# Performance work log

Measured on AMD Instinct MI355X. Metric: run time of the kernel, lower is better.

The kernel has to match this reference:

```python
import jax, jax.numpy as jnp
import numpy as np

N_NODES = 10000
N_EDGES = 320000
NODE_C = 256
IN_EDGE_C = 256
OUT_EDGE_C = 512
BN_EPS = 1e-5


def setup_inputs() -> dict:
    key = jax.random.key(0)
    ks = jax.random.split(key, 10)
    d_in = 2 * NODE_C + IN_EDGE_C  # 768
    x = jax.random.normal(ks[0], (N_NODES, NODE_C), dtype=jnp.float32)
    edge_index = jax.random.randint(ks[1], (2, N_EDGES), 0, N_NODES, dtype=jnp.int64)
    edge_attr = jax.random.normal(ks[2], (N_EDGES, IN_EDGE_C), dtype=jnp.float32)
    # MLP params (Linear stored as [in, out] for x @ W + b)
    W1 = jax.random.normal(ks[3], (d_in, OUT_EDGE_C), dtype=jnp.float32) / np.sqrt(d_in)
    b1 = jnp.zeros((OUT_EDGE_C,), dtype=jnp.float32)
    W2 = jax.random.normal(ks[4], (OUT_EDGE_C, OUT_EDGE_C), dtype=jnp.float32) / np.sqrt(OUT_EDGE_C)
    b2 = jnp.zeros((OUT_EDGE_C,), dtype=jnp.float32)
    # BatchNorm affine params
    gamma = jnp.ones((OUT_EDGE_C,), dtype=jnp.float32)
    beta = jnp.zeros((OUT_EDGE_C,), dtype=jnp.float32)
    return {"x": x, "edge_index": edge_index, "edge_attr": edge_attr,
            "W1": W1, "b1": b1, "W2": W2, "b2": b2,
            "gamma": gamma, "beta": beta}


def reference(x, edge_index, edge_attr, W1, b1, W2, b2, gamma, beta):
    src = edge_index[0]  # x_j (source / neighbor)
    dst = edge_index[1]  # x_i (target, aggregation index)
    x_i = x[dst]                                  # [E, node_c]
    x_j = x[src]                                  # [E, node_c]
    m = jnp.concatenate([x_i, x_j - x_i, edge_attr], axis=-1)  # [E, 2*node_c+edge_c]
    h = jax.nn.relu(m @ W1 + b1) @ W2 + b2        # per-edge MLP -> [E, out_c]
    out = jax.ops.segment_sum(h, dst, num_segments=x.shape[0])  # scatter-add -> [N, out_c]
    # BatchNorm1d (training-mode batch statistics, biased variance)
    mean = jnp.mean(out, axis=0)
    var = jnp.var(out, axis=0)
    y = (out - mean) * jax.lax.rsqrt(var + BN_EPS) * gamma + beta
    return jax.nn.relu(y)
```

## Files before the change

kernel.cpp:

```cpp
#include <hip/hip_runtime.h>
#include <hip/hip_bf16.h>
#include <cstdint>

#define NN 10000
#define NE 320000
#define NC 256
#define OC 512
#define K1 256

typedef __bf16 bf16_t;
typedef bf16_t bf16x8 __attribute__((ext_vector_type(8)));
typedef bf16_t bf16x4 __attribute__((ext_vector_type(4)));
typedef bf16_t bf16x2 __attribute__((ext_vector_type(2)));
typedef float  f32x4  __attribute__((ext_vector_type(4)));
typedef float  f32x2  __attribute__((ext_vector_type(2)));

__device__ __forceinline__ void gload_lds16(const void* g, void* l) {
  __builtin_amdgcn_global_load_lds(
      (const __attribute__((address_space(1))) unsigned int*)g,
      (__attribute__((address_space(3))) unsigned int*)l, 16, 0, 0);
}

__device__ __forceinline__ int permB(int R) {
  return (R & ~63) + ((R & 15) << 2) + ((R >> 4) & 3);
}
__device__ __forceinline__ int permB32(int R) {
  return (R & ~31) + ((R & 15) << 1) + ((R >> 4) & 1);
}

__global__ void k_prep(const float* __restrict__ x,
                       const float* __restrict__ W1,
                       const float* __restrict__ W2,
                       bf16_t* __restrict__ xb,
                       bf16_t* __restrict__ w1abt,
                       bf16_t* __restrict__ w1ct,
                       bf16_t* __restrict__ w2t,
                       float* __restrict__ agg,
                       int* __restrict__ deg,
                       int* __restrict__ cursor,
                       float* __restrict__ sums) {
  const int stride = gridDim.x * blockDim.x;
  for (int i = blockIdx.x * blockDim.x + threadIdx.x; i < NN * OC; i += stride) {
    agg[i] = 0.0f;
    if (i < NN * NC) xb[i] = (bf16_t)x[i];
    if (i < 1024 * K1) {
      const int n = i >> 8, k = i & 255;
      float w;
      if (n < OC) w = W1[(size_t)k * OC + n] - W1[(size_t)(k + NC) * OC + n];
      else        w = W1[(size_t)(k + NC) * OC + (n - OC)];
      w1abt[i] = (bf16_t)w;
    }
    if (i < OC * K1) {
      const int n = i >> 8, k = i & 255;
      w1ct[i] = (bf16_t)W1[(size_t)(512 + k) * OC + n];
    }
    if (i < OC * OC) {
      const int n = i >> 9, k = i & 511;
      w2t[i] = (bf16_t)W2[(size_t)k * OC + n];
    }
    if (i < NN) { deg[i] = 0; cursor[i] = 0; }
    if (i < 1024) sums[i] = 0.0f;
  }
}

__global__ void k_deg(const int* __restrict__ dstIdx, int* __restrict__ deg) {
  const int i = blockIdx.x * blockDim.x + threadIdx.x;
  if (i < NE) atomicAdd(&deg[dstIdx[i]], 1);
}

__global__ void k_scan(const int* __restrict__ deg, int* __restrict__ offs) {
  __shared__ int carry;
  __shared__ int wsum[4];
  if (threadIdx.x == 0) carry = 0;
  __syncthreads();
  const int lane = threadIdx.x & 63, w = threadIdx.x >> 6;
  for (int base = 0; base < NN; base += 256) {
    const int i = base + threadIdx.x;
    const int v = (i < NN) ? deg[i] : 0;
    int s = v;
#pragma unroll
    for (int d = 1; d < 64; d <<= 1) { int t = __shfl_up(s, d); if (lane >= d) s += t; }
    if (lane == 63) wsum[w] = s;
    __syncthreads();
    int woff = 0;
    for (int j = 0; j < w; j++) woff += wsum[j];
    const int incl = s + woff + carry;
    if (i < NN) offs[i] = incl - v;
    __syncthreads();
    if (threadIdx.x == 255) carry = incl;
    __syncthreads();
  }
}

__global__ void k_scatter(const int* __restrict__ srcIdx, const int* __restrict__ dstIdx,
                          const int* __restrict__ offs, int* __restrict__ cursor,
                          int* __restrict__ eperm, int* __restrict__ sdst,
                          int* __restrict__ ssrc) {
  const int e = blockIdx.x * blockDim.x + threadIdx.x;
  if (e < NE) {
    const int d = dstIdx[e];
    const int pos = offs[d] + atomicAdd(&cursor[d], 1);
    eperm[pos] = e;
    sdst[pos] = d;
    ssrc[pos] = srcIdx[e];
  }
}

__global__ __launch_bounds__(256) void k_pq(
    const bf16_t* __restrict__ xb,
    const bf16_t* __restrict__ w1abt,
    const float*  __restrict__ b1,
    float*        __restrict__ P,
    bf16_t*       __restrict__ Qb) {
  __shared__ bf16_t sA[128 * 64];
  __shared__ bf16_t sB[128 * 64];

  const int tid = threadIdx.x;
  const int cb = blockIdx.x & 7, rblk = blockIdx.x >> 3;
  const int r0 = rblk * 128, n0 = cb * 128;
  const int lane = tid & 63, wid = tid >> 6;
  const int mbase = (wid >> 1) * 64, nbase = (wid & 1) * 64;
  const int lr = lane >> 3, ls = lane & 7, slog = ls ^ lr;
  const int g = lane >> 4;

  f32x4 acc[4][4];
#pragma unroll
  for (int mi = 0; mi < 4; mi++)
#pragma unroll
    for (int ni = 0; ni < 4; ni++) acc[mi][ni] = (f32x4){0.f, 0.f, 0.f, 0.f};

  for (int kb = 0; kb < K1; kb += 64) {
#pragma unroll
    for (int i = 0; i < 4; i++) {
      const int row = wid * 32 + i * 8;
      int grow = r0 + row + lr;
      if (grow > NN - 1) grow = NN - 1;
      gload_lds16(xb + (size_t)grow * NC + kb + slog * 8, &sA[row * 64]);
      gload_lds16(w1abt + (size_t)(n0 + permB(row + lr)) * K1 + kb + slog * 8,
                  &sB[row * 64]);
    }
    __syncthreads();
#pragma unroll
    for (int kk = 0; kk < 2; kk++) {
      const int sl = kk * 4 + g;
      bf16x8 av[4], bv[4];
#pragma unroll
      for (int mi = 0; mi < 4; mi++) {
        const int rA = mbase + mi * 16 + (lane & 15);
        av[mi] = *(const bf16x8*)&sA[rA * 64 + ((sl ^ (rA & 7)) * 8)];
      }
#pragma unroll
      for (int ni = 0; ni < 4; ni++) {
        const int rB = nbase + ni * 16 + (lane & 15);
        bv[ni] = *(const bf16x8*)&sB[rB * 64 + ((sl ^ (rB & 7)) * 8)];
      }
#pragma unroll
      for (int mi = 0; mi < 4; mi++)
#pragma unroll
        for (int ni = 0; ni < 4; ni++)
          acc[mi][ni] = __builtin_amdgcn_mfma_f32_16x16x32_bf16(av[mi], bv[ni], acc[mi][ni], 0, 0, 0);
    }
    __syncthreads();
  }

  const int col0 = n0 + nbase + (lane & 15) * 4;
  f32x4 b1v = {0.f, 0.f, 0.f, 0.f};
  if (col0 < OC) b1v = *(const f32x4*)&b1[col0];
#pragma unroll
  for (int mi = 0; mi < 4; mi++) {
#pragma unroll
    for (int q = 0; q < 4; q++) {
      const int grow = r0 + mbase + mi * 16 + g * 4 + q;
      if (grow < NN) {
        if (col0 < OC) {
          f32x4 v;
#pragma unroll
          for (int j = 0; j < 4; j++) v[j] = acc[mi][j][q] + b1v[j];
          *(f32x4*)&P[(size_t)grow * OC + col0] = v;
        } else {
          bf16x4 v;
#pragma unroll
          for (int j = 0; j < 4; j++) v[j] = (bf16_t)acc[mi][j][q];
          *(bf16x4*)&Qb[(size_t)grow * OC + (col0 - OC)] = v;
        }
      }
    }
  }
}

__global__ __launch_bounds__(512, 4) void k_edge_gemm(
    const float*  __restrict__ ea,
    const bf16_t* __restrict__ w1ct,
    const float*  __restrict__ P,
    const bf16_t* __restrict__ Qb,
    const int*    __restrict__ eperm,
    const int*    __restrict__ sdst,
    const int*    __restrict__ ssrc,
    float*        __restrict__ agg) {
  __shared__ bf16_t sM[2][128 * 64];
  __shared__ bf16_t sW[2][128 * 64];
  __shared__ int sDst[128];
  __shared__ int sSrc[128];
  __shared__ int sE[128];

  const int bid = (blockIdx.x & 7) * 1250 + (blockIdx.x >> 3);
  const int cb = bid & 3, eblk = bid >> 2;
  const int e0 = eblk * 128, n0 = cb * 128;

  const int tid = threadIdx.x;
  if (tid < 128) {
    sDst[tid] = sdst[e0 + tid];
    sSrc[tid] = ssrc[e0 + tid];
    sE[tid]   = eperm[e0 + tid];
  }
  __syncthreads();

  const int lane = tid & 63, wid = tid >> 6;
  const int mbase = (wid >> 2) * 64;
  const int nbase = (wid & 3) * 32;
  const int g = lane >> 4, r = lane & 15;
  const int lr = lane >> 3, ls = lane & 7, slogW = ls ^ lr;
  const int mrow = tid >> 2, qd = tid & 3;
  const int msw = mrow & 7;
  const float* eaRow = ea + (size_t)sE[mrow] * NC;

#define STAGE_W(kt, b)                                                        \
  _Pragma("unroll") for (int i = 0; i < 2; i++) {                             \
    const int rowb = wid * 16 + i * 8;       \
    gload_lds16(w1ct + (size_t)(n0 + permB32(rowb + lr)) * K1 + (kt)*64 + slogW * 8, \
                &sW[b][rowb * 64]);                                           \
  }
#define LOAD_A(kt)                                                            \
  _Pragma("unroll") for (int j = 0; j < 4; j++)                               \
      a[j] = *(const f32x4*)(eaRow + (kt)*64 + qd * 16 + j * 4);
#define WRITE_M(b)                                                            \
  _Pragma("unroll") for (int tt = 0; tt < 2; tt++) {                          \
    const int slot = qd * 2 + tt;                                             \
    bf16x8 v;                                                                 \
    _Pragma("unroll") for (int jj = 0; jj < 4; jj++) {                        \
      v[jj] = (bf16_t)a[tt * 2][jj];                                          \
      v[4 + jj] = (bf16_t)a[tt * 2 + 1][jj];                                  \
    }                                                                         \
    *(bf16x8*)&sM[b][mrow * 64 + ((slot ^ msw) * 8)] = v;                     \
  }

  f32x4 a[4];
  STAGE_W(0, 0);
  LOAD_A(0);
  WRITE_M(0);

  f32x4 acc[4][2];
#pragma unroll
  for (int mi = 0; mi < 4; mi++)
#pragma unroll
    for (int ni = 0; ni < 2; ni++) acc[mi][ni] = (f32x4){0.f, 0.f, 0.f, 0.f};

#pragma unroll
  for (int t = 0; t < 4; t++) {
    const int b = t & 1;
    __syncthreads();
    if (t < 3) { STAGE_W(t + 1, b ^ 1); LOAD_A(t + 1); }
#pragma unroll
    for (int kk = 0; kk < 2; kk++) {
      const int sl = kk * 4 + g;
      bf16x8 av[4], bv[2];
#pragma unroll
      for (int mi = 0; mi < 4; mi++) {
        const int rA = mbase + mi * 16 + r;
        av[mi] = *(const bf16x8*)&sM[b][rA * 64 + ((sl ^ (rA & 7)) * 8)];
      }
#pragma unroll
      for (int ni = 0; ni < 2; ni++) {
        const int rB = nbase + ni * 16 + r;
        bv[ni] = *(const bf16x8*)&sW[b][rB * 64 + ((sl ^ (rB & 7)) * 8)];
      }
#pragma unroll
      for (int mi = 0; mi < 4; mi++)
#pragma unroll
        for (int ni = 0; ni < 2; ni++)
          acc[mi][ni] = __builtin_amdgcn_mfma_f32_16x16x32_bf16(av[mi], bv[ni], acc[mi][ni], 0, 0, 0);
    }
    if (t < 3) { WRITE_M(b ^ 1); }
  }
#undef STAGE_W
#undef LOAD_A
#undef WRITE_M

  const int col0 = n0 + nbase + r * 2;
#pragma unroll
  for (int mi = 0; mi < 4; mi++) {
    const int rbase = mbase + mi * 16 + g * 4;
    const int d0 = sDst[rbase],     d1 = sDst[rbase + 1];
    const int d2 = sDst[rbase + 2], d3 = sDst[rbase + 3];
    const int s0 = sSrc[rbase],     s1 = sSrc[rbase + 1];
    const int s2 = sSrc[rbase + 2], s3 = sSrc[rbase + 3];
    const int headId = d0, tailId = d3;
    const bool b1q = (d1 != d0), b2q = (d2 != d1), b3q = (d3 != d2);
    const bool seen = b1q | b2q | b3q;
    bool match[3];
#pragma unroll
    for (int j = 0; j < 3; j++) {
      const int tIdj = __shfl(tailId, (lane & 15) | (j << 4));
      match[j] = (j < g) && (tIdj == headId);
    }
    const int nextHead = __shfl(headId, (lane + 16) & 63);
    const bool endsHere = (g == 3) || (nextHead != tailId);

    const f32x2 P0 = *(const f32x2*)&P[(size_t)d0 * OC + col0];
    const f32x2 P1 = *(const f32x2*)&P[(size_t)d1 * OC + col0];
    const f32x2 P2 = *(const f32x2*)&P[(size_t)d2 * OC + col0];
    const f32x2 P3 = *(const f32x2*)&P[(size_t)d3 * OC + col0];
    const bf16x2 Q0 = *(const bf16x2*)&Qb[(size_t)s0 * OC + col0];
    const bf16x2 Q1 = *(const bf16x2*)&Qb[(size_t)s1 * OC + col0];
    const bf16x2 Q2 = *(const bf16x2*)&Qb[(size_t)s2 * OC + col0];
    const bf16x2 Q3 = *(const bf16x2*)&Qb[(size_t)s3 * OC + col0];

    f32x2 v0, v1, v2, v3;
#pragma unroll
    for (int j = 0; j < 2; j++) {
      v0[j] = fmaxf(acc[mi][j][0] + P0[j] + (float)Q0[j], 0.f);
      v1[j] = fmaxf(acc[mi][j][1] + P1[j] + (float)Q1[j], 0.f);
      v2[j] = fmaxf(acc[mi][j][2] + P2[j] + (float)Q2[j], 0.f);
      v3[j] = fmaxf(acc[mi][j][3] + P3[j] + (float)Q3[j], 0.f);
    }

    f32x2 head = {0.f, 0.f}, run = v0;
    bool first = true;
    if (b1q) { head = run; first = false; run = v1; } else run += v1;
    if (b2q) {
      if (first) { head = run; first = false; }
      else {
        float* base = agg + (size_t)d1 * OC + col0;
#pragma unroll
        for (int j = 0; j < 2; j++) if (run[j] != 0.f) atomicAdd(base + j, run[j]);
      }
      run = v2;
    } else run += v2;
    if (b3q) {
      if (first) { head = run; first = false; }
      else {
        float* base = agg + (size_t)d2 * OC + col0;
#pragma unroll
        for (int j = 0; j < 2; j++) if (run[j] != 0.f) atomicAdd(base + j, run[j]);
      }
      run = v3;
    } else run += v3;
    const f32x2 tailSum = run;

    f32x2 inc = {0.f, 0.f};
#pragma unroll
    for (int jg = 0; jg < 3; jg++) {
      f32x2 ts;
#pragma unroll
      for (int c = 0; c < 2; c++) ts[c] = __shfl(tailSum[c], (lane & 15) | (jg << 4));
      if (match[jg]) inc += ts;
    }
    if (seen) {
      float* base = agg + (size_t)headId * OC + col0;
#pragma unroll
      for (int j = 0; j < 2; j++) {
        const float h = head[j] + inc[j];
        if (h != 0.f) atomicAdd(base + j, h);
      }
    }
    if (endsHere) {
      float* base = agg + (size_t)tailId * OC + col0;
#pragma unroll
      for (int j = 0; j < 2; j++) {
        const float t2 = tailSum[j] + (seen ? 0.f : inc[j]);
        if (t2 != 0.f) atomicAdd(base + j, t2);
      }
    }
  }
}

__global__ __launch_bounds__(256) void k_node_gemm(
    const float*  __restrict__ agg,
    const bf16_t* __restrict__ w2t,
    const float*  __restrict__ b2,
    const int*    __restrict__ deg,
    float*        __restrict__ out,
    float*        __restrict__ sums) {
  __shared__ bf16_t sM[128 * 72];
  __shared__ bf16_t sW[128 * 72];

  const int tid  = threadIdx.x;
  const int bid  = blockIdx.x;
  const int cb   = bid & 3;
  const int rblk = bid >> 2;
  const int r0   = rblk * 128;
  const int n0   = cb * 128;

  const int lane  = tid & 63, wid = tid >> 6;
  const int mbase = (wid >> 1) * 64, nbase = (wid & 1) * 64;
  const int se = tid >> 1;
  const int sk = (tid & 1) * 32;
  const int arow  = r0 + se;
  const bool rowok = arow < NN;

  f32x4 acc[4][4];
#pragma unroll
  for (int mi = 0; mi < 4; mi++)
#pragma unroll
    for (int ni = 0; ni < 4; ni++) acc[mi][ni] = (f32x4){0.f, 0.f, 0.f, 0.f};

  for (int kb = 0; kb < OC; kb += 64) {
    {
      bf16x8* dst = (bf16x8*)&sM[se * 72 + sk];
      if (rowok) {
        const float* pf = agg + (size_t)arow * OC + kb + sk;
        f32x4 f[8];
#pragma unroll
        for (int i = 0; i < 8; i++) f[i] = *(const f32x4*)(pf + i * 4);
#pragma unroll
        for (int i = 0; i < 4; i++) {
          bf16x8 v;
#pragma unroll
          for (int j = 0; j < 4; j++) {
            v[j]     = (bf16_t)f[2 * i][j];
            v[4 + j] = (bf16_t)f[2 * i + 1][j];
          }
          dst[i] = v;
        }
      } else {
        bf16x8 z = {};
        dst[0] = z; dst[1] = z; dst[2] = z; dst[3] = z;
      }
    }
    {
      const bf16_t* pw = w2t + (size_t)(n0 + permB(se)) * OC + kb + sk;
      bf16x8* dst = (bf16x8*)&sW[se * 72 + sk];
      dst[0] = *(const bf16x8*)(pw);
      dst[1] = *(const bf16x8*)(pw + 8);
      dst[2] = *(const bf16x8*)(pw + 16);
      dst[3] = *(const bf16x8*)(pw + 24);
    }
    __syncthreads();
#pragma unroll
    for (int kk = 0; kk < 2; kk++) {
      const int krd = kk * 32 + (lane >> 4) * 8;
      bf16x8 av[4], bv[4];
#pragma unroll
      for (int mi = 0; mi < 4; mi++)
        av[mi] = *(const bf16x8*)&sM[(mbase + mi * 16 + (lane & 15)) * 72 + krd];
#pragma unroll
      for (int ni = 0; ni < 4; ni++)
        bv[ni] = *(const bf16x8*)&sW[(nbase + ni * 16 + (lane & 15)) * 72 + krd];
#pragma unroll
      for (int mi = 0; mi < 4; mi++)
#pragma unroll
        for (int ni = 0; ni < 4; ni++)
          acc[mi][ni] = __builtin_amdgcn_mfma_f32_16x16x32_bf16(av[mi], bv[ni], acc[mi][ni], 0, 0, 0);
    }
    __syncthreads();
  }

  const int col0 = n0 + nbase + (lane & 15) * 4;
  const f32x4 b2v = *(const f32x4*)&b2[col0];
  const int g = lane >> 4;
  f32x4 s1 = {0.f, 0.f, 0.f, 0.f}, s2 = {0.f, 0.f, 0.f, 0.f};
#pragma unroll
  for (int mi = 0; mi < 4; mi++) {
#pragma unroll
    for (int q = 0; q < 4; q++) {
      const int row = r0 + mbase + mi * 16 + g * 4 + q;
      if (row < NN) {
        const float dg = (float)deg[row];
        f32x4 v;
#pragma unroll
        for (int j = 0; j < 4; j++) {
          v[j] = acc[mi][j][q] + b2v[j] * dg;
          s1[j] += v[j];
          s2[j] += v[j] * v[j];
        }
        *(f32x4*)&out[(size_t)row * OC + col0] = v;
      }
    }
  }
#pragma unroll
  for (int j = 0; j < 4; j++) {
    s1[j] += __shfl_xor(s1[j], 16);  s2[j] += __shfl_xor(s2[j], 16);
    s1[j] += __shfl_xor(s1[j], 32);  s2[j] += __shfl_xor(s2[j], 32);
  }
  if (g == 0) {
#pragma unroll
    for (int j = 0; j < 4; j++) {
      atomicAdd(&sums[col0 + j], s1[j]);
      atomicAdd(&sums[OC + col0 + j], s2[j]);
    }
  }
}

__global__ void k_bn_apply(float* __restrict__ out,
                           const float* __restrict__ sums,
                           const float* __restrict__ gamma,
                           const float* __restrict__ beta) {
  const int i = blockIdx.x * blockDim.x + threadIdx.x;
  f32x4 v = *((const f32x4*)out + i);
  const int c = (i & 127) << 2;
  const f32x4 sm = *(const f32x4*)&sums[c];
  const f32x4 sq = *(const f32x4*)&sums[OC + c];
  const f32x4 gm = *(const f32x4*)&gamma[c];
  const f32x4 bt = *(const f32x4*)&beta[c];
  f32x4 r;
#pragma unroll
  for (int j = 0; j < 4; j++) {
    const float mean = sm[j] * (1.0f / NN);
    const float var  = sq[j] * (1.0f / NN) - mean * mean;
    const float sc   = rsqrtf(var + 1e-5f) * gm[j];
    r[j] = fmaxf(v[j] * sc + (bt[j] - mean * sc), 0.0f);
  }
  *((f32x4*)out + i) = r;
}

extern "C" void kernel_launch(void* const* d_in, const int* in_sizes, int n_in,
                              void* d_out, int out_size, void* d_ws, size_t ws_size,
                              hipStream_t stream) {
  const float* x     = (const float*)d_in[0];
  const int*   ei    = (const int*)d_in[1];
  const float* ea    = (const float*)d_in[2];
  const float* W1    = (const float*)d_in[3];
  const float* b1    = (const float*)d_in[4];
  const float* W2    = (const float*)d_in[5];
  const float* b2    = (const float*)d_in[6];
  const float* gamma = (const float*)d_in[7];
  const float* beta  = (const float*)d_in[8];
  float* out = (float*)d_out;

  char* ws = (char*)d_ws;
  float*  agg    = (float*)(ws);
  float*  P      = (float*)(ws + 20480000);
  bf16_t* Qb     = (bf16_t*)(ws + 40960000);
  bf16_t* xb     = (bf16_t*)(ws + 51200000);
  bf16_t* w1abt  = (bf16_t*)(ws + 56320000);
  bf16_t* w1ct   = (bf16_t*)(ws + 56844288);
  bf16_t* w2t    = (bf16_t*)(ws + 57106432);
  int*    deg    = (int*)(ws + 57630720);
  int*    offs   = (int*)(ws + 57670720);
  int*    cursor = (int*)(ws + 57710720);
  float*  sums   = (float*)(ws + 57750720);
  int*    eperm  = (int*)(ws + 57754816);
  int*    sdst   = (int*)(ws + 59034816);
  int*    ssrc   = (int*)(ws + 60314816);

  const int* srcIdx = ei;
  const int* dstIdx = ei + NE;

  k_prep<<<4096, 256, 0, stream>>>(x, W1, W2, xb, w1abt, w1ct, w2t, agg, deg, cursor, sums);
  k_deg<<<(NE + 255) / 256, 256, 0, stream>>>(dstIdx, deg);
  k_scan<<<1, 256, 0, stream>>>(deg, offs);
  k_scatter<<<(NE + 255) / 256, 256, 0, stream>>>(srcIdx, dstIdx, offs, cursor,
                                                  eperm, sdst, ssrc);
  k_pq<<<((NN + 127) / 128) * 8, 256, 0, stream>>>(xb, w1abt, b1, P, Qb);
  k_edge_gemm<<<(NE / 128) * 4, 512, 0, stream>>>(ea, w1ct, P, Qb, eperm, sdst, ssrc, agg);
  k_node_gemm<<<((NN + 127) / 128) * 4, 256, 0, stream>>>(agg, w2t, b2, deg, out, sums);
  k_bn_apply<<<(NN * OC / 4 + 255) / 256, 256, 0, stream>>>(out, sums, gamma, beta);
}
```

Before: 424.8 us.

## Double edge-GEMM block threads and move buffer zeroing to hipMemsetAsync

```diff
diff --git a/kernel.cpp b/kernel.cpp
--- a/kernel.cpp
+++ b/kernel.cpp
@@ -34,15 +34,10 @@
                        bf16_t* __restrict__ xb,
                        bf16_t* __restrict__ w1abt,
                        bf16_t* __restrict__ w1ct,
-                       bf16_t* __restrict__ w2t,
-                       float* __restrict__ agg,
-                       int* __restrict__ deg,
-                       int* __restrict__ cursor,
-                       float* __restrict__ sums) {
+                       bf16_t* __restrict__ w2t) {
   const int stride = gridDim.x * blockDim.x;
-  for (int i = blockIdx.x * blockDim.x + threadIdx.x; i < NN * OC; i += stride) {
-    agg[i] = 0.0f;
-    if (i < NN * NC) xb[i] = (bf16_t)x[i];
+  for (int i = blockIdx.x * blockDim.x + threadIdx.x; i < NN * NC; i += stride) {
+    xb[i] = (bf16_t)x[i];
     if (i < 1024 * K1) {
       const int n = i >> 8, k = i & 255;
       float w;
@@ -58,8 +53,6 @@
       const int n = i >> 9, k = i & 511;
       w2t[i] = (bf16_t)W2[(size_t)k * OC + n];
     }
-    if (i < NN) { deg[i] = 0; cursor[i] = 0; }
-    if (i < 1024) sums[i] = 0.0f;
   }
 }
 
@@ -188,7 +181,7 @@
   }
 }
 
-__global__ __launch_bounds__(512, 4) void k_edge_gemm(
+__global__ __launch_bounds__(1024, 8) void k_edge_gemm(
     const float*  __restrict__ ea,
     const bf16_t* __restrict__ w1ct,
     const float*  __restrict__ P,
@@ -216,42 +209,43 @@
   __syncthreads();
 
   const int lane = tid & 63, wid = tid >> 6;
-  const int mbase = (wid >> 2) * 64;
+  const int mbase = (wid >> 2) * 32;
   const int nbase = (wid & 3) * 32;
   const int g = lane >> 4, r = lane & 15;
   const int lr = lane >> 3, ls = lane & 7, slogW = ls ^ lr;
-  const int mrow = tid >> 2, qd = tid & 3;
+  const int mrow = tid >> 3, qd = tid & 7;
   const int msw = mrow & 7;
   const float* eaRow = ea + (size_t)sE[mrow] * NC;
 
 #define STAGE_W(kt, b)                                                        \
-  _Pragma("unroll") for (int i = 0; i < 2; i++) {                             \
-    const int rowb = wid * 16 + i * 8;       \
+  {                                                                           \
+    const int rowb = wid * 8;      \
     gload_lds16(w1ct + (size_t)(n0 + permB32(rowb + lr)) * K1 + (kt)*64 + slogW * 8, \
                 &sW[b][rowb * 64]);                                           \
   }
 #define LOAD_A(kt)                                                            \
-  _Pragma("unroll") for (int j = 0; j < 4; j++)                               \
-      a[j] = *(const f32x4*)(eaRow + (kt)*64 + qd * 16 + j * 4);
+  {                                                                           \
+    a[0] = *(const f32x4*)(eaRow + (kt)*64 + qd * 8);                         \
+    a[1] = *(const f32x4*)(eaRow + (kt)*64 + qd * 8 + 4);                     \
+  }
 #define WRITE_M(b)                                                            \
-  _Pragma("unroll") for (int tt = 0; tt < 2; tt++) {                          \
-    const int slot = qd * 2 + tt;                                             \
+  {                                                                           \
     bf16x8 v;                                                                 \
     _Pragma("unroll") for (int jj = 0; jj < 4; jj++) {                        \
-      v[jj] = (bf16_t)a[tt * 2][jj];                                          \
-      v[4 + jj] = (bf16_t)a[tt * 2 + 1][jj];                                  \
+      v[jj]     = (bf16_t)a[0][jj];                                           \
+      v[4 + jj] = (bf16_t)a[1][jj];                                           \
     }                                                                         \
-    *(bf16x8*)&sM[b][mrow * 64 + ((slot ^ msw) * 8)] = v;                     \
-  }
-
-  f32x4 a[4];
+    *(bf16x8*)&sM[b][mrow * 64 + ((qd ^ msw) * 8)] = v;                       \
+  }
+
+  f32x4 a[2];
   STAGE_W(0, 0);
   LOAD_A(0);
   WRITE_M(0);
 
-  f32x4 acc[4][2];
-#pragma unroll
-  for (int mi = 0; mi < 4; mi++)
+  f32x4 acc[2][2];
+#pragma unroll
+  for (int mi = 0; mi < 2; mi++)
 #pragma unroll
     for (int ni = 0; ni < 2; ni++) acc[mi][ni] = (f32x4){0.f, 0.f, 0.f, 0.f};
 
@@ -263,9 +257,9 @@
 #pragma unroll
     for (int kk = 0; kk < 2; kk++) {
       const int sl = kk * 4 + g;
-      bf16x8 av[4], bv[2];
-#pragma unroll
-      for (int mi = 0; mi < 4; mi++) {
+      bf16x8 av[2], bv[2];
+#pragma unroll
+      for (int mi = 0; mi < 2; mi++) {
         const int rA = mbase + mi * 16 + r;
         av[mi] = *(const bf16x8*)&sM[b][rA * 64 + ((sl ^ (rA & 7)) * 8)];
       }
@@ -275,7 +269,7 @@
         bv[ni] = *(const bf16x8*)&sW[b][rB * 64 + ((sl ^ (rB & 7)) * 8)];
       }
 #pragma unroll
-      for (int mi = 0; mi < 4; mi++)
+      for (int mi = 0; mi < 2; mi++)
 #pragma unroll
         for (int ni = 0; ni < 2; ni++)
           acc[mi][ni] = __builtin_amdgcn_mfma_f32_16x16x32_bf16(av[mi], bv[ni], acc[mi][ni], 0, 0, 0);
@@ -288,7 +282,7 @@
 
   const int col0 = n0 + nbase + r * 2;
 #pragma unroll
-  for (int mi = 0; mi < 4; mi++) {
+  for (int mi = 0; mi < 2; mi++) {
     const int rbase = mbase + mi * 16 + g * 4;
     const int d0 = sDst[rbase],     d1 = sDst[rbase + 1];
     const int d2 = sDst[rbase + 2], d3 = sDst[rbase + 3];
@@ -546,13 +540,16 @@
   const int* srcIdx = ei;
   const int* dstIdx = ei + NE;
 
-  k_prep<<<4096, 256, 0, stream>>>(x, W1, W2, xb, w1abt, w1ct, w2t, agg, deg, cursor, sums);
+  hipMemsetAsync(agg, 0, 20480000, stream);
+  hipMemsetAsync(deg, 0, 124096, stream);
+
+  k_prep<<<4096, 256, 0, stream>>>(x, W1, W2, xb, w1abt, w1ct, w2t);
   k_deg<<<(NE + 255) / 256, 256, 0, stream>>>(dstIdx, deg);
   k_scan<<<1, 256, 0, stream>>>(deg, offs);
   k_scatter<<<(NE + 255) / 256, 256, 0, stream>>>(srcIdx, dstIdx, offs, cursor,
                                                   eperm, sdst, ssrc);
   k_pq<<<((NN + 127) / 128) * 8, 256, 0, stream>>>(xb, w1abt, b1, P, Qb);
-  k_edge_gemm<<<(NE / 128) * 4, 512, 0, stream>>>(ea, w1ct, P, Qb, eperm, sdst, ssrc, agg);
+  k_edge_gemm<<<(NE / 128) * 4, 1024, 0, stream>>>(ea, w1ct, P, Qb, eperm, sdst, ssrc, agg);
   k_node_gemm<<<((NN + 127) / 128) * 4, 256, 0, stream>>>(agg, w2t, b2, deg, out, sums);
   k_bn_apply<<<(NN * OC / 4 + 255) / 256, 256, 0, stream>>>(out, sums, gamma, beta);
 }
```

After: 452.3 us. 6.5% more time.
